# Performance work log

Measured on AMD Instinct MI355X. Metric: run time of the kernel, lower is better.

Reference implementation:

```python
import jax, jax.numpy as jnp
import numpy as np

B, S, D, H = 2, 2048, 1024, 16
HD = D // H          # head dim = 64
BASE = 10000.0
SCALE = 1.0 / np.sqrt(HD)


def setup_inputs() -> dict:
    key = jax.random.key(0)
    ks = jax.random.split(key, 7)
    mk = lambda k, shp: (jax.random.normal(k, shp, dtype=jnp.float32) * 0.02)
    return {
        "hidden_states": jax.random.normal(ks[0], (B, S, D), dtype=jnp.float32),
        "Wq": mk(ks[1], (D, D)), "bq": jnp.zeros((D,), jnp.float32),
        "Wk": mk(ks[2], (D, D)), "bk": jnp.zeros((D,), jnp.float32),
        "Wv": mk(ks[3], (D, D)), "bv": jnp.zeros((D,), jnp.float32),
    }


def _rope_tables(seq_len, head_dim, dtype):
    # Intended RoPE: inv_freq over head_dim/2 frequencies.
    # (Original torch code has an off-by-2 indexing bug that makes it un-runnable
    #  for head_dim > 2; we implement the intended standard RoPE:
    #  inv_freq = base^{-arange(0, head_dim, 2)/head_dim}, length head_dim//2.)
    dim_half = head_dim // 2
    inv_freq = 1.0 / (BASE ** (jnp.arange(dim_half, dtype=dtype) / dim_half))
    ang = jnp.arange(seq_len, dtype=dtype)[:, None] * inv_freq[None, :]  # [S, dim_half]
    return jnp.sin(ang), jnp.cos(ang)


def _apply_rope(x, sin, cos):
    # x: [B, H, S, HD]; sin/cos: [S, HD//2]
    dim_half = x.shape[-1] // 2
    x1, x2 = x[..., :dim_half], x[..., dim_half:]
    sin = sin[None, None]  # [1,1,S,dim_half]
    cos = cos[None, None]
    return jnp.concatenate([x1 * cos - x2 * sin, x1 * sin + x2 * cos], axis=-1)


def reference(hidden_states, Wq, bq, Wk, bk, Wv, bv):
    b, s, d = hidden_states.shape
    # QKV projections (nn.Linear: x @ W.T + b), then split heads -> [B,H,S,HD]
    def proj(W, bias):
        y = jnp.einsum("bsd,ed->bse", hidden_states, W) + bias
        return y.reshape(b, s, H, HD).transpose(0, 2, 1, 3)

    q, k, v = proj(Wq, bq), proj(Wk, bk), proj(Wv, bv)

    sin, cos = _rope_tables(s, HD, hidden_states.dtype)
    q = _apply_rope(q, sin, cos)
    k = _apply_rope(k, sin, cos)

    # Non-causal SDPA, scale = 1/sqrt(head_dim), no mask, eval mode (no dropout)
    scores = jnp.einsum("bhqd,bhkd->bhqk", q, k) * SCALE
    probs = jax.nn.softmax(scores, axis=-1)
    ctx = jnp.einsum("bhqk,bhkd->bhqd", probs, v)

    # [B,H,S,HD] -> [B,S,D]
    return ctx.transpose(0, 2, 1, 3).reshape(b, s, d)
```

## Files before the change

kernel.cpp:

```cpp
#include <hip/hip_runtime.h>
#include <hip/hip_bf16.h>
#include <math.h>

#define B_  2
#define S_  2048
#define D_  1024
#define H_  16
#define HD_ 64
#define M_  (B_*S_)
#define N3  (3*D_)
#define K_  D_
#define LOG2E 1.44269504088896340736f

typedef unsigned short u16;
typedef __bf16 bf16x8 __attribute__((ext_vector_type(8)));
typedef float  f32x4  __attribute__((ext_vector_type(4)));
typedef unsigned short u16x4 __attribute__((ext_vector_type(4)));
typedef unsigned short u16x8 __attribute__((ext_vector_type(8)));

typedef const __attribute__((address_space(1))) unsigned int gu32;
typedef __attribute__((address_space(3)))       unsigned int lu32;

__device__ __forceinline__ void gload_lds16(const void* g, void* l) {
  __builtin_amdgcn_global_load_lds((gu32*)g, (lu32*)l, 16, 0, 0);
}

__device__ __forceinline__ u16 f2bf(float f) {
  unsigned u = __builtin_bit_cast(unsigned, f);
  u += 0x7fffu + ((u >> 16) & 1u);
  return (u16)(u >> 16);
}

__global__ void k_prep(const float* __restrict__ hs, const float* __restrict__ Wq,
                       const float* __restrict__ Wk, const float* __restrict__ Wv,
                       u16* __restrict__ Xb, u16* __restrict__ Wb) {
  const int NX = M_*D_/4, NW = D_*D_/4;
  int i = blockIdx.x * blockDim.x + threadIdx.x;
  const float4* src; u16* dst; int off;
  if (i < NX)            { src = (const float4*)hs; dst = Xb;           off = i; }
  else if (i < NX+NW)    { src = (const float4*)Wq; dst = Wb;           off = i-NX; }
  else if (i < NX+2*NW)  { src = (const float4*)Wk; dst = Wb + D_*D_;   off = i-NX-NW; }
  else                   { src = (const float4*)Wv; dst = Wb + 2*D_*D_; off = i-NX-2*NW; }
  float4 v = src[off];
  ushort4 o; o.x = f2bf(v.x); o.y = f2bf(v.y); o.z = f2bf(v.z); o.w = f2bf(v.w);
  reinterpret_cast<ushort4*>(dst)[off] = o;
}

__global__ void k_tables(float* __restrict__ sinT, float* __restrict__ cosT) {
  int gid = blockIdx.x * blockDim.x + threadIdx.x;
  int s = gid >> 5, j = gid & 31;
  float invf = (float)exp(-(double)j * (log(10000.0) / 32.0));
  float angf = (float)s * invf;
  double ang = (double)angf;
  sinT[gid] = (float)sin(ang);
  cosT[gid] = (float)cos(ang);
}

#define BM 128
#define BN 128
#define BK 64

__global__ __launch_bounds__(256) void k_gemm(const u16* __restrict__ A,
                                              const u16* __restrict__ Bm,
                                              const float* __restrict__ bq,
                                              const float* __restrict__ bk,
                                              const float* __restrict__ bv,
                                              const float* __restrict__ sinT,
                                              const float* __restrict__ cosT,
                                              u16* __restrict__ Qo,
                                              u16* __restrict__ Ko,
                                              u16* __restrict__ Vo) {
  __shared__ alignas(16) u16 As[BM*BK];
  __shared__ alignas(16) u16 Bs[BN*BK];
  const int t = threadIdx.x;
  const int l = t & 63, w = t >> 6;
  const int wr = w >> 1, wc = w & 1;
  const int lr = l & 15, lg = l >> 4;
  const int m0 = blockIdx.y * BM, n0 = blockIdx.x * BN;

  f32x4 acc[4][4] = {};

  for (int k0 = 0; k0 < K_; k0 += BK) {
#pragma unroll
    for (int i = 0; i < 4; ++i) {
      int chunk = i*256 + t;
      int row = chunk >> 3, kc = chunk & 7;
      gload_lds16(A + (size_t)(m0+row)*K_ + k0 + kc*8, &As[chunk*8]);
    }
#pragma unroll
    for (int i = 0; i < 4; ++i) {
      int chunk = i*256 + t;
      int row = chunk >> 3, kc = chunk & 7;
      gload_lds16(Bm + (size_t)(n0+row)*K_ + k0 + kc*8, &Bs[chunk*8]);
    }
    __syncthreads();
#pragma unroll
    for (int ks = 0; ks < 2; ++ks) {
      bf16x8 a[4], b[4];
#pragma unroll
      for (int m = 0; m < 4; ++m)
        a[m] = *reinterpret_cast<const bf16x8*>(&As[(wr*64 + m*16 + lr)*BK + ks*32 + lg*8]);
#pragma unroll
      for (int n = 0; n < 4; ++n)
        b[n] = *reinterpret_cast<const bf16x8*>(&Bs[(wc*64 + n*16 + lr)*BK + ks*32 + lg*8]);
#pragma unroll
      for (int m = 0; m < 4; ++m)
#pragma unroll
        for (int n = 0; n < 4; ++n)
          acc[m][n] = __builtin_amdgcn_mfma_f32_16x16x32_bf16(a[m], b[n], acc[m][n], 0, 0, 0);
    }
    __syncthreads();
  }

  const int cw0  = n0 + wc*64;
  const int proj = cw0 >> 10;
  const int h    = (cw0 & (D_-1)) >> 6;
  const int b    = m0 >> 11;
  const int sb_  = (m0 & (S_-1)) + wr*64;

  if (proj < 2) {
    const float* bias = proj ? bk : bq;
    u16* dst = proj ? Ko : Qo;
    const float qs = proj ? 1.0f : 0.125f * LOG2E;
    float b1[2], b2[2];
#pragma unroll
    for (int n = 0; n < 2; ++n) {
      b1[n] = bias[h*HD_ + n*16 + lr];
      b2[n] = bias[h*HD_ + n*16 + lr + 32];
    }
#pragma unroll
    for (int m = 0; m < 4; ++m)
#pragma unroll
      for (int r = 0; r < 4; ++r) {
        int s = sb_ + m*16 + lg*4 + r;
        size_t orow = ((size_t)(b*H_ + h)*S_ + s)*HD_;
#pragma unroll
        for (int n = 0; n < 2; ++n) {
          int j = n*16 + lr;
          float x1 = acc[m][n][r]   + b1[n];
          float x2 = acc[m][n+2][r] + b2[n];
          float c  = cosT[(s<<5) + j], sn = sinT[(s<<5) + j];
          dst[orow + j]      = f2bf((x1*c - x2*sn) * qs);
          dst[orow + j + 32] = f2bf((x1*sn + x2*c) * qs);
        }
      }
  } else {
    float bb[4];
#pragma unroll
    for (int n = 0; n < 4; ++n) bb[n] = bv[h*HD_ + n*16 + lr];
#pragma unroll
    for (int m = 0; m < 4; ++m)
#pragma unroll
      for (int r = 0; r < 4; ++r) {
        int s = sb_ + m*16 + lg*4 + r;
        size_t orow = ((size_t)(b*H_ + h)*S_ + s)*HD_;
#pragma unroll
        for (int n = 0; n < 4; ++n)
          Vo[orow + n*16 + lr] = f2bf(acc[m][n][r] + bb[n]);
      }
  }
}

__global__ __launch_bounds__(256) void k_vt2(const u16* __restrict__ Vb,
                                             u16* __restrict__ Vt) {
  __shared__ u16 tile[64*68];
  const int bh = blockIdx.y, s0 = blockIdx.x * 64, t = threadIdx.x;
#pragma unroll
  for (int i = 0; i < 2; ++i) {
    int chunk = i*256 + t;
    int sl = chunk >> 3, c8 = chunk & 7;
    u16x8 v = *reinterpret_cast<const u16x8*>(Vb + ((size_t)bh*S_ + s0 + sl)*HD_ + c8*8);
    u16x4 lo = __builtin_shufflevector(v, v, 0, 1, 2, 3);
    u16x4 hi = __builtin_shufflevector(v, v, 4, 5, 6, 7);
    *reinterpret_cast<u16x4*>(&tile[sl*68 + c8*8])     = lo;
    *reinterpret_cast<u16x4*>(&tile[sl*68 + c8*8 + 4]) = hi;
  }
  __syncthreads();
#pragma unroll
  for (int i = 0; i < 2; ++i) {
    int chunk = i*256 + t;
    int hd = chunk >> 3, sb = chunk & 7;
    u16x8 o;
#pragma unroll
    for (int k = 0; k < 8; ++k) o[k] = tile[(sb*8 + k)*68 + hd];
    *reinterpret_cast<u16x8*>(Vt + ((size_t)bh*HD_ + hd)*S_ + s0 + sb*8) = o;
  }
}

#define QT 128
#define KT 64
#define NT (S_/KT)

__global__ __launch_bounds__(512) void k_attn(const u16* __restrict__ Q,
                                              const u16* __restrict__ K,
                                              const u16* __restrict__ Vt,
                                              float* __restrict__ out) {
  __shared__ alignas(16) u16 Ks[2][KT*HD_];
  __shared__ alignas(16) u16 Vs[2][HD_*KT];
  __shared__ alignas(16) u16 Ps[QT*KT];
  const int t = threadIdx.x, l = t & 63, w = t >> 6;
  const int lr = l & 15, lg = l >> 4;

  const int bid = blockIdx.x;
  const int work = (bid & 7) * 64 + (bid >> 3);
  const int bh = work >> 4;
  const int q0 = (work & 15) * QT;

  const u16* Qg = Q  + ((size_t)bh*S_ + q0)*HD_;
  const u16* Kg = K  + (size_t)bh*S_*HD_;
  const u16* Vg = Vt + (size_t)bh*HD_*S_;

  bf16x8 aq[2];
#pragma unroll
  for (int ks = 0; ks < 2; ++ks)
    aq[ks] = *reinterpret_cast<const bf16x8*>(Qg + (size_t)(w*16 + lr)*HD_ + ks*32 + lg*8);

  f32x4 O[4] = {};
  float lsum[4] = {};

  const int srow = t >> 3, sg = t & 7;
  const int sgK = sg ^ (srow & 7);

  gload_lds16(Kg + (size_t)srow*HD_ + sgK*8, &Ks[0][t*8]);
  gload_lds16(Vg + (size_t)srow*S_  + sgK*8, &Vs[0][t*8]);
  __syncthreads();

  int cur = 0;
  for (int kt = 0; kt < NT; ++kt) {
    if (kt + 1 < NT) {
      gload_lds16(Kg + (size_t)(kt+1)*KT*HD_ + (size_t)srow*HD_ + sgK*8, &Ks[cur^1][t*8]);
      gload_lds16(Vg + (size_t)srow*S_ + (kt+1)*KT + sgK*8,              &Vs[cur^1][t*8]);
    }

    f32x4 sf[4] = {};
    __builtin_amdgcn_s_setprio(1);
#pragma unroll
    for (int ks = 0; ks < 2; ++ks) {
#pragma unroll
      for (int n = 0; n < 4; ++n) {
        int krow = n*16 + lr;
        bf16x8 bk_ = *reinterpret_cast<const bf16x8*>(
            &Ks[cur][krow*HD_ + (((ks<<2) + lg) ^ (krow & 7))*8]);
        sf[n] = __builtin_amdgcn_mfma_f32_16x16x32_bf16(aq[ks], bk_, sf[n], 0, 0, 0);
      }
    }
    __builtin_amdgcn_s_setprio(0);

#pragma unroll
    for (int n = 0; n < 4; ++n)
#pragma unroll
      for (int r = 0; r < 4; ++r) {
        float p = exp2f(sf[n][r]);
        lsum[r] += p;
        int prow = w*16 + lg*4 + r;
        int pg   = (n*2 + (lr >> 3)) ^ (prow & 7);
        Ps[prow*KT + pg*8 + (lr & 7)] = f2bf(p);
      }

    __builtin_amdgcn_s_setprio(1);
#pragma unroll
    for (int ks = 0; ks < 2; ++ks) {
      int arow = w*16 + lr;
      bf16x8 ap = *reinterpret_cast<const bf16x8*>(
          &Ps[arow*KT + (((ks<<2) + lg) ^ (arow & 7))*8]);
#pragma unroll
      for (int n = 0; n < 4; ++n) {
        int vrow = n*16 + lr;
        bf16x8 bv_ = *reinterpret_cast<const bf16x8*>(
            &Vs[cur][vrow*KT + (((ks<<2) + lg) ^ (vrow & 7))*8]);
        O[n] = __builtin_amdgcn_mfma_f32_16x16x32_bf16(ap, bv_, O[n], 0, 0, 0);
      }
    }
    __builtin_amdgcn_s_setprio(0);

    __syncthreads();
    cur ^= 1;
  }

#pragma unroll
  for (int r = 0; r < 4; ++r) {
    float rs = lsum[r];
    rs += __shfl_xor(rs, 1); rs += __shfl_xor(rs, 2);
    rs += __shfl_xor(rs, 4); rs += __shfl_xor(rs, 8);
    lsum[r] = rs;
  }

  const int b = bh >> 4, h = bh & 15;
#pragma unroll
  for (int r = 0; r < 4; ++r) {
    float inv = 1.f / lsum[r];
    int sr = q0 + w*16 + lg*4 + r;
#pragma unroll
    for (int n = 0; n < 4; ++n)
      out[(size_t)(b*S_ + sr)*D_ + h*HD_ + n*16 + lr] = O[n][r] * inv;
  }
}

extern "C" void kernel_launch(void* const* d_in, const int* in_sizes, int n_in,
                              void* d_out, int out_size, void* d_ws, size_t ws_size,
                              hipStream_t stream) {
  const float* hs = (const float*)d_in[0];
  const float* Wq = (const float*)d_in[1];
  const float* bq = (const float*)d_in[2];
  const float* Wk = (const float*)d_in[3];
  const float* bk = (const float*)d_in[4];
  const float* Wv = (const float*)d_in[5];
  const float* bv = (const float*)d_in[6];
  float* out = (float*)d_out;

  char* ws = (char*)d_ws;
  u16*   Xb   = (u16*)  (ws);
  u16*   Wb   = (u16*)  (ws + 8388608);
  u16*   Qb   = (u16*)  (ws + 14680064);
  u16*   Kb   = (u16*)  (ws + 23068672);
  u16*   Vb   = (u16*)  (ws + 31457280);
  u16*   Vtb  = (u16*)  (ws + 39845888);
  float* sinT = (float*)(ws + 48234496);
  float* cosT = (float*)(ws + 48496640);

  k_prep<<<(M_*D_/4 + 3*(D_*D_/4)) / 256, 256, 0, stream>>>(hs, Wq, Wk, Wv, Xb, Wb);
  k_tables<<<256, 256, 0, stream>>>(sinT, cosT);
  k_gemm<<<dim3(N3/BN, M_/BM), 256, 0, stream>>>(Xb, Wb, bq, bk, bv, sinT, cosT, Qb, Kb, Vb);
  k_vt2<<<dim3(S_/64, B_*H_), 256, 0, stream>>>(Vb, Vtb);
  k_attn<<<512, 512, 0, stream>>>(Qb, Kb, Vtb, out);
}
```

Measured before the change: 207.8 us.

## Switch attention to 32x32 MFMA with register-resident probabilities, drop LDS P staging

The attention kernel moves from 16x16x32 to 32x32x16 bf16 MFMA and computes S^T = K·Q^T, so the exponentiated scores land in registers already laid out as the A operand of the PV product. This removes the shared-memory round trip for P and the per-row shuffle reduction. Each wave now handles 32 query rows, so the block covers 256 queries and the grid is halved to 256 blocks. To match the new register layout, the V transpose kernel permutes key order within 16-key groups. The cost is fewer blocks in flight and larger accumulators per wave.

Measured after the change: 204.9 us. About the same (-1.4%).

```diff
diff --git a/kernel.cpp b/kernel.cpp
--- a/kernel.cpp
+++ b/kernel.cpp
@@ -15,8 +15,10 @@
 typedef unsigned short u16;
 typedef __bf16 bf16x8 __attribute__((ext_vector_type(8)));
 typedef float  f32x4  __attribute__((ext_vector_type(4)));
+typedef float  f32x16 __attribute__((ext_vector_type(16)));
 typedef unsigned short u16x4 __attribute__((ext_vector_type(4)));
 typedef unsigned short u16x8 __attribute__((ext_vector_type(8)));
+typedef unsigned int   u32x4v __attribute__((ext_vector_type(4)));
 
 typedef const __attribute__((address_space(1))) unsigned int gu32;
 typedef __attribute__((address_space(3)))       unsigned int lu32;
@@ -29,6 +31,12 @@
   unsigned u = __builtin_bit_cast(unsigned, f);
   u += 0x7fffu + ((u >> 16) & 1u);
   return (u16)(u >> 16);
+}
+
+__device__ __forceinline__ unsigned pk2(float lo, float hi) {
+  unsigned d;
+  asm("v_cvt_pk_bf16_f32 %0, %1, %2" : "=v"(d) : "v"(lo), "v"(hi));
+  return d;
 }
 
 __global__ void k_prep(const float* __restrict__ hs, const float* __restrict__ Wq,
@@ -182,41 +190,47 @@
     int hd = chunk >> 3, sb = chunk & 7;
     u16x8 o;
 #pragma unroll
-    for (int k = 0; k < 8; ++k) o[k] = tile[(sb*8 + k)*68 + hd];
+    for (int k = 0; k < 8; ++k) {
+      int p   = sb*8 + k;
+      int key = (p & ~15) | (p & 3) | ((p & 4) << 1) | ((p & 8) >> 1);
+      o[k] = tile[key*68 + hd];
+    }
     *reinterpret_cast<u16x8*>(Vt + ((size_t)bh*HD_ + hd)*S_ + s0 + sb*8) = o;
   }
 }
 
-#define QT 128
-#define KT 64
-#define NT (S_/KT)
+#define QBW 32
+#define NWV 8
+#define QTT (QBW*NWV)
+#define KTL 64
+#define NTL (S_/KTL)
 
 __global__ __launch_bounds__(512) void k_attn(const u16* __restrict__ Q,
                                               const u16* __restrict__ K,
                                               const u16* __restrict__ Vt,
                                               float* __restrict__ out) {
-  __shared__ alignas(16) u16 Ks[2][KT*HD_];
-  __shared__ alignas(16) u16 Vs[2][HD_*KT];
-  __shared__ alignas(16) u16 Ps[QT*KT];
+  __shared__ alignas(16) u16 Ks[2][KTL*HD_];
+  __shared__ alignas(16) u16 Vs[2][HD_*KTL];
+  __shared__ float lsums[NWV][QBW];
   const int t = threadIdx.x, l = t & 63, w = t >> 6;
-  const int lr = l & 15, lg = l >> 4;
+  const int q32 = l & 31, hi = l >> 5;
 
   const int bid = blockIdx.x;
-  const int work = (bid & 7) * 64 + (bid >> 3);
-  const int bh = work >> 4;
-  const int q0 = (work & 15) * QT;
-
-  const u16* Qg = Q  + ((size_t)bh*S_ + q0)*HD_;
+  const int work = (bid & 7) * 32 + (bid >> 3);
+  const int bh = work >> 3;
+  const int q0 = (work & 7) * QTT;
+
+  const u16* Qg = Q  + ((size_t)bh*S_ + q0 + w*QBW)*HD_;
   const u16* Kg = K  + (size_t)bh*S_*HD_;
   const u16* Vg = Vt + (size_t)bh*HD_*S_;
 
-  bf16x8 aq[2];
-#pragma unroll
-  for (int ks = 0; ks < 2; ++ks)
-    aq[ks] = *reinterpret_cast<const bf16x8*>(Qg + (size_t)(w*16 + lr)*HD_ + ks*32 + lg*8);
-
-  f32x4 O[4] = {};
-  float lsum[4] = {};
+  bf16x8 qf[4];
+#pragma unroll
+  for (int kt = 0; kt < 4; ++kt)
+    qf[kt] = *reinterpret_cast<const bf16x8*>(Qg + (size_t)q32*HD_ + kt*16 + hi*8);
+
+  f32x16 O0 = {}, O1 = {};
+  float lsum = 0.f;
 
   const int srow = t >> 3, sg = t & 7;
   const int sgK = sg ^ (srow & 7);
@@ -226,50 +240,48 @@
   __syncthreads();
 
   int cur = 0;
-  for (int kt = 0; kt < NT; ++kt) {
-    if (kt + 1 < NT) {
-      gload_lds16(Kg + (size_t)(kt+1)*KT*HD_ + (size_t)srow*HD_ + sgK*8, &Ks[cur^1][t*8]);
-      gload_lds16(Vg + (size_t)srow*S_ + (kt+1)*KT + sgK*8,              &Vs[cur^1][t*8]);
-    }
-
-    f32x4 sf[4] = {};
+  for (int tile = 0; tile < NTL; ++tile) {
+    if (tile + 1 < NTL) {
+      gload_lds16(Kg + ((size_t)(tile+1)*KTL + srow)*HD_ + sgK*8, &Ks[cur^1][t*8]);
+      gload_lds16(Vg + (size_t)srow*S_ + (tile+1)*KTL + sgK*8,    &Vs[cur^1][t*8]);
+    }
+
+    f32x16 d0 = {}, d1 = {};
     __builtin_amdgcn_s_setprio(1);
 #pragma unroll
-    for (int ks = 0; ks < 2; ++ks) {
-#pragma unroll
-      for (int n = 0; n < 4; ++n) {
-        int krow = n*16 + lr;
-        bf16x8 bk_ = *reinterpret_cast<const bf16x8*>(
-            &Ks[cur][krow*HD_ + (((ks<<2) + lg) ^ (krow & 7))*8]);
-        sf[n] = __builtin_amdgcn_mfma_f32_16x16x32_bf16(aq[ks], bk_, sf[n], 0, 0, 0);
+    for (int kt = 0; kt < 4; ++kt) {
+      const int gsw = ((kt*2 + hi) ^ (q32 & 7)) * 8;
+      bf16x8 k0 = *reinterpret_cast<const bf16x8*>(&Ks[cur][q32*HD_ + gsw]);
+      d0 = __builtin_amdgcn_mfma_f32_32x32x16_bf16(k0, qf[kt], d0, 0, 0, 0);
+      bf16x8 k1 = *reinterpret_cast<const bf16x8*>(&Ks[cur][(32 + q32)*HD_ + gsw]);
+      d1 = __builtin_amdgcn_mfma_f32_32x32x16_bf16(k1, qf[kt], d1, 0, 0, 0);
+    }
+    __builtin_amdgcn_s_setprio(0);
+
+    unsigned pw[4][4];
+#pragma unroll
+    for (int c = 0; c < 4; ++c) {
+      float e[8];
+#pragma unroll
+      for (int i = 0; i < 8; ++i) {
+        float sv = (c < 2) ? d0[(c & 1)*8 + i] : d1[(c & 1)*8 + i];
+        e[i] = exp2f(sv);
+        lsum += e[i];
       }
-    }
-    __builtin_amdgcn_s_setprio(0);
-
-#pragma unroll
-    for (int n = 0; n < 4; ++n)
-#pragma unroll
-      for (int r = 0; r < 4; ++r) {
-        float p = exp2f(sf[n][r]);
-        lsum[r] += p;
-        int prow = w*16 + lg*4 + r;
-        int pg   = (n*2 + (lr >> 3)) ^ (prow & 7);
-        Ps[prow*KT + pg*8 + (lr & 7)] = f2bf(p);
-      }
+#pragma unroll
+      for (int j = 0; j < 4; ++j) pw[c][j] = pk2(e[2*j], e[2*j+1]);
+    }
 
     __builtin_amdgcn_s_setprio(1);
 #pragma unroll
-    for (int ks = 0; ks < 2; ++ks) {
-      int arow = w*16 + lr;
-      bf16x8 ap = *reinterpret_cast<const bf16x8*>(
-          &Ps[arow*KT + (((ks<<2) + lg) ^ (arow & 7))*8]);
-#pragma unroll
-      for (int n = 0; n < 4; ++n) {
-        int vrow = n*16 + lr;
-        bf16x8 bv_ = *reinterpret_cast<const bf16x8*>(
-            &Vs[cur][vrow*KT + (((ks<<2) + lg) ^ (vrow & 7))*8]);
-        O[n] = __builtin_amdgcn_mfma_f32_16x16x32_bf16(ap, bv_, O[n], 0, 0, 0);
-      }
+    for (int c = 0; c < 4; ++c) {
+      u32x4v pv_ = {pw[c][0], pw[c][1], pw[c][2], pw[c][3]};
+      bf16x8 pa = __builtin_bit_cast(bf16x8, pv_);
+      const int gv = ((c*2 + hi) ^ (q32 & 7)) * 8;
+      bf16x8 v0 = *reinterpret_cast<const bf16x8*>(&Vs[cur][q32*KTL + gv]);
+      O0 = __builtin_amdgcn_mfma_f32_32x32x16_bf16(pa, v0, O0, 0, 0, 0);
+      bf16x8 v1 = *reinterpret_cast<const bf16x8*>(&Vs[cur][(32 + q32)*KTL + gv]);
+      O1 = __builtin_amdgcn_mfma_f32_32x32x16_bf16(pa, v1, O1, 0, 0, 0);
     }
     __builtin_amdgcn_s_setprio(0);
 
@@ -277,22 +289,17 @@
     cur ^= 1;
   }
 
-#pragma unroll
-  for (int r = 0; r < 4; ++r) {
-    float rs = lsum[r];
-    rs += __shfl_xor(rs, 1); rs += __shfl_xor(rs, 2);
-    rs += __shfl_xor(rs, 4); rs += __shfl_xor(rs, 8);
-    lsum[r] = rs;
-  }
+  lsum += __shfl_xor(lsum, 32);
+  if (l < 32) lsums[w][l] = lsum;
 
   const int b = bh >> 4, h = bh & 15;
 #pragma unroll
-  for (int r = 0; r < 4; ++r) {
-    float inv = 1.f / lsum[r];
-    int sr = q0 + w*16 + lg*4 + r;
-#pragma unroll
-    for (int n = 0; n < 4; ++n)
-      out[(size_t)(b*S_ + sr)*D_ + h*HD_ + n*16 + lr] = O[n][r] * inv;
+  for (int r = 0; r < 16; ++r) {
+    int qrow = (r & 3) + 8*(r >> 2) + 4*hi;
+    float inv = 1.f / lsums[w][qrow];
+    size_t o = (size_t)(b*S_ + q0 + w*QBW + qrow)*D_ + h*HD_;
+    out[o + q32]      = O0[r] * inv;
+    out[o + 32 + q32] = O1[r] * inv;
   }
 }
 
@@ -322,5 +329,5 @@
   k_tables<<<256, 256, 0, stream>>>(sinT, cosT);
   k_gemm<<<dim3(N3/BN, M_/BM), 256, 0, stream>>>(Xb, Wb, bq, bk, bv, sinT, cosT, Qb, Kb, Vb);
   k_vt2<<<dim3(S_/64, B_*H_), 256, 0, stream>>>(Vb, Vtb);
-  k_attn<<<512, 512, 0, stream>>>(Qb, Kb, Vtb, out);
-}
+  k_attn<<<256, 512, 0, stream>>>(Qb, Kb, Vtb, out);
+}
```
